# Optimization experiments

Hardware: AMD Instinct MI355X
Metric: run time of the kernel (lower is better)

Reference implementation:

```python
import jax, jax.numpy as jnp
import numpy as np

B, H, N, D, C, G = 4, 4, 4096, 256, 256, 64  # batch, heads, tokens, emb, channels, grid
EPS = 1e-5


def _layernorm(x, g, b):
    mu = jnp.mean(x, axis=-1, keepdims=True)
    var = jnp.var(x, axis=-1, keepdims=True)
    return (x - mu) * jax.lax.rsqrt(var + EPS) * g + b


def setup_inputs() -> dict:
    key = jax.random.key(0)
    ks = jax.random.split(key, 24)
    s = lambda fan_in: 1.0 / np.sqrt(fan_in)
    inp = {
        "img_emb": jax.random.normal(ks[0], (B, C, G, G), jnp.float32),
        "point_emb": jax.random.normal(ks[1], (B, N, D), jnp.float32),
        # stacked per-head projections (torch Linear: y = x @ W.T + b; store W already transposed)
        "Wq": jax.random.uniform(ks[2], (H, D, D), jnp.float32, -s(D), s(D)),
        "bq": jax.random.uniform(ks[3], (H, D), jnp.float32, -s(D), s(D)),
        "Wk": jax.random.uniform(ks[4], (H, C, D), jnp.float32, -s(C), s(C)),
        "bk": jax.random.uniform(ks[5], (H, D), jnp.float32, -s(C), s(C)),
        "Wv": jax.random.uniform(ks[6], (H, C, D), jnp.float32, -s(C), s(C)),
        "bv": jax.random.uniform(ks[7], (H, D), jnp.float32, -s(C), s(C)),
        "Wo": jax.random.uniform(ks[8], (H * D, D), jnp.float32, -s(H * D), s(H * D)),
        "bo": jax.random.uniform(ks[9], (D,), jnp.float32, -s(H * D), s(H * D)),
        "pos": jax.random.normal(ks[10], (N, D), jnp.float32),
        # FF: 256->128->64->1
        "W1": jax.random.uniform(ks[11], (256, 128), jnp.float32, -s(256), s(256)),
        "b1": jax.random.uniform(ks[12], (128,), jnp.float32, -s(256), s(256)),
        "g1": jnp.ones((128,), jnp.float32),
        "be1": jnp.zeros((128,), jnp.float32),
        "W2": jax.random.uniform(ks[13], (128, 64), jnp.float32, -s(128), s(128)),
        "b2": jax.random.uniform(ks[14], (64,), jnp.float32, -s(128), s(128)),
        "g2": jnp.ones((64,), jnp.float32),
        "be2": jnp.zeros((64,), jnp.float32),
        "W3": jax.random.uniform(ks[15], (64, 1), jnp.float32, -s(64), s(64)),
        "b3": jax.random.uniform(ks[16], (1,), jnp.float32, -s(64), s(64)),
    }
    return inp


def reference(img_emb, point_emb, Wq, bq, Wk, bk, Wv, bv, Wo, bo, pos,
              W1, b1, g1, be1, W2, b2, g2, be2, W3, b3):
    b = img_emb.shape[0]
    # [B, C, G, G] -> [B, N, C]
    img = jnp.transpose(img_emb, (0, 2, 3, 1)).reshape(b, -1, img_emb.shape[1])
    img_pos = img + pos[None, :, :]
    # batched per-head QKV (collapses the per-head Python loop)
    q = jnp.einsum('bnd,hde->bhne', point_emb, Wq) + bq[None, :, None, :]
    k = jnp.einsum('bnc,hce->bhne', img, Wk) + bk[None, :, None, :]
    v = jnp.einsum('bnc,hce->bhne', img_pos, Wv) + bv[None, :, None, :]
    scores = jnp.einsum('bhqe,bhke->bhqk', q, k) / jnp.sqrt(jnp.float32(D))
    attn = jax.nn.softmax(scores, axis=-1)
    att = jnp.einsum('bhqk,bhke->bhqe', attn, v)          # [B, H, N, E]
    att = jnp.transpose(att, (0, 2, 1, 3)).reshape(b, N, H * D)  # concat heads
    emb = att @ Wo + bo + point_emb                        # residual, [B, N, D]
    # small FFN head
    h = _layernorm(jax.nn.relu(emb @ W1 + b1), g1, be1)
    h = _layernorm(jax.nn.relu(h @ W2 + b2), g2, be2)
    act = jax.nn.sigmoid(h @ W3 + b3)                      # [B, N, 1]
    return act, emb
```

## Files before the change

### kernel.cpp

```cpp
#include <hip/hip_runtime.h>

typedef __attribute__((ext_vector_type(8))) short bfrag;
typedef __attribute__((ext_vector_type(8))) unsigned short us8;
typedef __attribute__((ext_vector_type(16))) float f16v;

__device__ __forceinline__ unsigned short f2bf(float f) {
  union { float f; unsigned u; } v; v.f = f;
  unsigned u = v.u;
  return (unsigned short)((u + 0x7fffu + ((u >> 16) & 1u)) >> 16);
}
__device__ __forceinline__ unsigned pkbf(float a, float b) {
  return (unsigned)f2bf(a) | ((unsigned)f2bf(b) << 16);
}
__device__ __forceinline__ float wred(float v) {
#pragma unroll
  for (int m = 32; m >= 1; m >>= 1) v += __shfl_xor(v, m, 64);
  return v;
}
__device__ __forceinline__ void dma16(const void* g, void* l) {
  __builtin_amdgcn_global_load_lds(
      (const __attribute__((address_space(1))) void*)g,
      (__attribute__((address_space(3))) void*)l, 16, 0, 0);
}

__device__ __forceinline__ void transp64(
    const float* __restrict__ inz, unsigned short* __restrict__ oz,
    int R, int Cc, int i0, int j0, int tid)
{
  int l = tid & 63, ty = tid >> 6;
  int i = i0 + l;
#pragma unroll
  for (int itr = 0; itr < 2; ++itr) {
    int j = j0 + ty * 16 + itr * 8;
    const float* p = inz + (long)i * Cc + j;
    float4 v0 = *(const float4*)(p);
    float4 v1 = *(const float4*)(p + 4);
    float vv[8] = {v0.x, v0.y, v0.z, v0.w, v1.x, v1.y, v1.z, v1.w};
#pragma unroll
    for (int s = 0; s < 8; ++s) oz[(long)(j + s) * R + i] = f2bf(vv[s]);
  }
}

__global__ __launch_bounds__(256) void prep_kernel(
    const float* __restrict__ point_emb, short* __restrict__ peT,
    const float* __restrict__ img_emb, const float* __restrict__ pos,
    short* __restrict__ imgT, short* __restrict__ imgPosT,
    const float* __restrict__ Wq, const float* __restrict__ Wk,
    const float* __restrict__ Wv, short* __restrict__ WqT,
    const float* __restrict__ Wo, short* __restrict__ WoT)
{
  __shared__ float tile[64][65];
  int b = blockIdx.x;
  int tid = threadIdx.x;

  if (b < 2048) {
    long i = ((long)b * 256 + tid) * 8;
    float4 v0 = *(const float4*)(point_emb + i);
    float4 v1 = *(const float4*)(point_emb + i + 4);
    uint4 st;
    st.x = pkbf(v0.x, v0.y);
    st.y = pkbf(v0.z, v0.w);
    st.z = pkbf(v1.x, v1.y);
    st.w = pkbf(v1.z, v1.w);
    *(uint4*)((unsigned short*)peT + i) = st;
  } else if (b < 3072) {
    int bb = b - 2048;
    int x = bb & 63, y = (bb >> 6) & 3, z = bb >> 8;
    long zofs = (long)z * (256L * 4096L);
    const float* inz = img_emb + zofs;
    int i0 = y * 64, j0 = x * 64;
    int r0 = (tid >> 6) * 16, c = tid & 63;
#pragma unroll
    for (int rr = 0; rr < 16; ++rr) {
      tile[c][r0 + rr] = inz[(long)(i0 + r0 + rr) * 4096 + j0 + c];
    }
    __syncthreads();
    unsigned short* o1 = (unsigned short*)imgT + zofs;
    unsigned short* o2 = (unsigned short*)imgPosT + zofs;
#pragma unroll
    for (int rr = 0; rr < 16; ++rr) {
      int tt = r0 + rr;
      float v = tile[tt][c];
      long o = (long)(j0 + tt) * 256 + i0 + c;
      o1[o] = f2bf(v);
      o2[o] = f2bf(v + pos[o]);
    }
  } else if (b < 3264) {
    int bb = b - 3072;
    int x = bb & 3, y = (bb >> 2) & 3, z = bb >> 4;
    const float* inz = (z < 4 ? Wq : (z < 8 ? Wk : Wv)) + (long)(z & 3) * 65536;
    unsigned short* oz = (unsigned short*)WqT + (long)z * 65536;
    transp64(inz, oz, 256, 256, x * 64, y * 64, tid);
  } else {
    int bb = b - 3264;
    int x = bb & 15, y = bb >> 4;
    transp64(Wo, (unsigned short*)WoT, 1024, 256, x * 64, y * 64, tid);
  }
}

__global__ __launch_bounds__(256) void gemm_qkv(
    const short* __restrict__ A, const short* __restrict__ Bt,
    const float* __restrict__ bias, short* __restrict__ Co,
    float scale, int transC)
{
  int id = blockIdx.x;
  int y = id & 3, h = (id >> 2) & 3;
  int g = id >> 4;
  int xt = g & 31, bsel = g >> 5;
  int z = bsel * 4 + h;

  const short* Az = A + (long)bsel * 1048576;
  const short* Btz = Bt + (long)h * 65536;
  const float* biasz = bias + (long)h * 256;
  short* Cz = Co + (long)z * 1048576;

  int tid = threadIdx.x;
  int w = tid >> 6, lane = tid & 63;
  int half = lane >> 5, ln = lane & 31;
  int wm = w & 1, wn = w >> 1;
  int row0 = xt * 128 + wm * 64;
  int col0 = y * 64 + wn * 32;

  f16v acc0, acc1;
#pragma unroll
  for (int i = 0; i < 16; ++i) { acc0[i] = 0.f; acc1[i] = 0.f; }

  const short* ap0 = Az + (long)(row0 + ln) * 256 + half * 8;
  const short* ap1 = Az + (long)(row0 + 32 + ln) * 256 + half * 8;
  const short* bp  = Btz + (long)(col0 + ln) * 256 + half * 8;

#pragma unroll
  for (int kt = 0; kt < 16; ++kt) {
    bfrag a0 = *(const bfrag*)(ap0 + kt * 16);
    bfrag a1 = *(const bfrag*)(ap1 + kt * 16);
    bfrag bb = *(const bfrag*)(bp + kt * 16);
    acc0 = __builtin_amdgcn_mfma_f32_32x32x16_bf16(a0, bb, acc0, 0, 0, 0);
    acc1 = __builtin_amdgcn_mfma_f32_32x32x16_bf16(a1, bb, acc1, 0, 0, 0);
  }

  int col = col0 + ln;
  float bv = biasz[col];
  if (transC) {
#pragma unroll
    for (int t = 0; t < 2; ++t) {
      int rbase = row0 + t * 32;
#pragma unroll
      for (int g2 = 0; g2 < 4; ++g2) {
        float v0 = ((t ? acc1[4*g2+0] : acc0[4*g2+0]) + bv) * scale;
        float v1 = ((t ? acc1[4*g2+1] : acc0[4*g2+1]) + bv) * scale;
        float v2 = ((t ? acc1[4*g2+2] : acc0[4*g2+2]) + bv) * scale;
        float v3 = ((t ? acc1[4*g2+3] : acc0[4*g2+3]) + bv) * scale;
        uint2 st;
        st.x = pkbf(v0, v1);
        st.y = pkbf(v2, v3);
        *(uint2*)&((unsigned short*)Cz)[(long)col * 4096 + rbase + 8 * g2 + 4 * half] = st;
      }
    }
  } else {
#pragma unroll
    for (int t = 0; t < 2; ++t) {
      int rbase = row0 + t * 32;
#pragma unroll
      for (int r = 0; r < 16; ++r) {
        float av = t ? acc1[r] : acc0[r];
        int rr = rbase + (r & 3) + 8 * (r >> 2) + 4 * half;
        ((unsigned short*)Cz)[(long)rr * 256 + col] = f2bf((av + bv) * scale);
      }
    }
  }
}

__global__ __launch_bounds__(256) void gemm_out(
    const short* __restrict__ A, const short* __restrict__ Bt,
    const float* __restrict__ bias, float* __restrict__ Co,
    const float* __restrict__ resid)
{
  int id = blockIdx.x;
  int xt = id >> 2, y = id & 3;

  int tid = threadIdx.x;
  int w = tid >> 6, lane = tid & 63;
  int half = lane >> 5, ln = lane & 31;
  int wm = w & 1, wn = w >> 1;
  int row0 = xt * 128 + wm * 64;
  int col0 = y * 64 + wn * 32;

  f16v acc0, acc1;
#pragma unroll
  for (int i = 0; i < 16; ++i) { acc0[i] = 0.f; acc1[i] = 0.f; }

  int r0 = row0 + ln, r1 = row0 + 32 + ln;
  long a0base = (long)(r0 >> 12) * 4194304 + (long)(r0 & 4095) * 256 + half * 8;
  long a1base = (long)(r1 >> 12) * 4194304 + (long)(r1 & 4095) * 256 + half * 8;
  const short* bp = Bt + (long)(col0 + ln) * 1024 + half * 8;

  for (int kh = 0; kh < 4; ++kh) {
    const short* a0p = A + a0base + (long)kh * 1048576;
    const short* a1p = A + a1base + (long)kh * 1048576;
    const short* bkp = bp + kh * 256;
#pragma unroll
    for (int kt = 0; kt < 16; ++kt) {
      bfrag a0 = *(const bfrag*)(a0p + kt * 16);
      bfrag a1 = *(const bfrag*)(a1p + kt * 16);
      bfrag bb = *(const bfrag*)(bkp + kt * 16);
      acc0 = __builtin_amdgcn_mfma_f32_32x32x16_bf16(a0, bb, acc0, 0, 0, 0);
      acc1 = __builtin_amdgcn_mfma_f32_32x32x16_bf16(a1, bb, acc1, 0, 0, 0);
    }
  }

  int col = col0 + ln;
  float bv = bias[col];
#pragma unroll
  for (int t = 0; t < 2; ++t) {
    int rbase = row0 + t * 32;
#pragma unroll
    for (int r = 0; r < 16; ++r) {
      float av = t ? acc1[r] : acc0[r];
      int rr = rbase + (r & 3) + 8 * (r >> 2) + 4 * half;
      Co[(long)rr * 256 + col] = av + bv + resid[(long)rr * 256 + col];
    }
  }
}

__global__ __launch_bounds__(512, 2) void attn_kernel(
    const short* __restrict__ Qg, const short* __restrict__ Kg,
    const short* __restrict__ Vtg, short* __restrict__ attc)
{
  __shared__ char smem[65536];
  int bx = blockIdx.x;
  int bh = bx & 15, qg = bx >> 4;
  int tid = threadIdx.x;
  int w = tid >> 6, lane = tid & 63;
  int half = lane >> 5, ln = lane & 31;
  int q0 = qg * 256 + w * 32;

  bfrag qf[16];
  {
    const short* qrow = Qg + ((long)bh * 4096 + q0 + ln) * 256 + half * 8;
#pragma unroll
    for (int kt = 0; kt < 16; ++kt) qf[kt] = *(const bfrag*)(qrow + kt * 16);
  }

  int koff[4], voff[2];
#pragma unroll
  for (int m = 0; m < 4; ++m) koff[m] = ((ln ^ (2 * m + half)) * 16) + half * 512;
#pragma unroll
  for (int kp = 0; kp < 2; ++kp) {
    int ck = 2 * kp + half;
    voff[kp] = 16384 + ck * 4096 + ((ln ^ (ck << 1)) * 16);
  }

  int w2 = w * 2;
  int kgl0, kgl1, vgl0, vgl1;
  {
    int c0 = w2 * 2 + half;
    kgl0 = (ln ^ (c0 & 7)) * 512 + c0 * 16;
    int c1 = (w2 + 1) * 2 + half;
    kgl1 = (ln ^ (c1 & 7)) * 512 + c1 * 16;
    int ck0 = w2 >> 2;
    int e0 = ((w2 & 3) * 64 + lane) ^ (ck0 << 1);
    vgl0 = e0 * 8192 + ck0 * 16;
    int ck1 = (w2 + 1) >> 2;
    int e1 = (((w2 + 1) & 3) * 64 + lane) ^ (ck1 << 1);
    vgl1 = e1 * 8192 + ck1 * 16;
  }
  const char* kgp = (const char*)Kg + (long)bh * 2097152;
  const char* vgp = (const char*)Vtg + (long)bh * 2097152;

  f16v O[8];
#pragma unroll
  for (int t = 0; t < 8; ++t)
#pragma unroll
    for (int r = 0; r < 16; ++r) O[t][r] = 0.f;

  float l_run = 0.f;
  union { bfrag f; unsigned u[4]; } bb[2];

#define PACK_BB(kp)                                                            \
  {                                                                            \
    unsigned q0_, q1_, q2_, q3_;                                               \
    asm("v_cvt_pk_bf16_f32 %0, %1, %2"                                         \
        : "=v"(q0_) : "v"(S[8*(kp)+0]), "v"(S[8*(kp)+1]));                     \
    asm("v_cvt_pk_bf16_f32 %0, %1, %2"                                         \
        : "=v"(q1_) : "v"(S[8*(kp)+2]), "v"(S[8*(kp)+3]));                     \
    asm("v_cvt_pk_bf16_f32 %0, %1, %2"                                         \
        : "=v"(q2_) : "v"(S[8*(kp)+4]), "v"(S[8*(kp)+5]));                     \
    asm("v_cvt_pk_bf16_f32 %0, %1, %2"                                         \
        : "=v"(q3_) : "v"(S[8*(kp)+6]), "v"(S[8*(kp)+7]));                     \
    asm("v_permlane32_swap_b32 %0, %1" : "+v"(q0_), "+v"(q2_));                \
    asm("v_permlane32_swap_b32 %0, %1" : "+v"(q1_), "+v"(q3_));                \
    bb[kp].u[0] = q0_;                                                         \
    bb[kp].u[1] = q1_;                                                         \
    bb[kp].u[2] = q2_;                                                         \
    bb[kp].u[3] = q3_;                                                         \
  }

  dma16(kgp + kgl0, smem + w2 * 1024);
  dma16(kgp + kgl1, smem + (w2 + 1) * 1024);
  kgp += 16384;

  __syncthreads();
  dma16(kgp + kgl0, smem + 32768 + w2 * 1024);
  dma16(kgp + kgl1, smem + 32768 + (w2 + 1) * 1024);
  kgp += 16384;
  dma16(vgp + vgl0, smem + 32768 + 16384 + w2 * 1024);
  dma16(vgp + vgl1, smem + 32768 + 16384 + (w2 + 1) * 1024);
  vgp += 64;
  {
    f16v S;
#pragma unroll
    for (int r = 0; r < 16; ++r) S[r] = 0.f;
#pragma unroll
    for (int kt = 0; kt < 16; ++kt) {
      bfrag a = *(const bfrag*)(smem + koff[kt & 3] + kt * 1024);
      S = __builtin_amdgcn_mfma_f32_32x32x16_bf16(a, qf[kt], S, 0, 0, 0);
    }
    float ss = 0.f;
#pragma unroll
    for (int r = 0; r < 16; ++r) { float e = exp2f(S[r] - 8.f); S[r] = e; ss += e; }
    l_run += ss;
    PACK_BB(0)
    PACK_BB(1)
  }

#define ATTN_ITER(BUF, KLOAD)                                                  \
  {                                                                            \
    __syncthreads();                                                           \
    if (KLOAD) {                                                               \
      dma16(kgp + kgl0, smem + ((BUF) ^ 1) * 32768 + w2 * 1024);               \
      dma16(kgp + kgl1, smem + ((BUF) ^ 1) * 32768 + (w2 + 1) * 1024);         \
      kgp += 16384;                                                            \
    }                                                                          \
    dma16(vgp + vgl0, smem + ((BUF) ^ 1) * 32768 + 16384 + w2 * 1024);         \
    dma16(vgp + vgl1, smem + ((BUF) ^ 1) * 32768 + 16384 + (w2 + 1) * 1024);   \
    vgp += 64;                                                                 \
    f16v S;                                                                    \
    _Pragma("unroll")                                                          \
    for (int r = 0; r < 16; ++r) S[r] = 0.f;                                   \
    _Pragma("unroll")                                                          \
    for (int kt = 0; kt < 16; ++kt) {                                          \
      bfrag a = *(const bfrag*)(smem + koff[kt & 3] + ((BUF)*32768 + kt*1024));\
      S = __builtin_amdgcn_mfma_f32_32x32x16_bf16(a, qf[kt], S, 0, 0, 0);      \
      bfrag va = *(const bfrag*)(smem + voff[kt >> 3] +                        \
                                 ((BUF)*32768 + (kt & 7) * 512));              \
      O[kt & 7] = __builtin_amdgcn_mfma_f32_32x32x16_bf16(va, bb[kt >> 3].f,   \
                                                          O[kt & 7], 0, 0, 0); \
    }                                                                          \
    float ss = 0.f;                                                            \
    _Pragma("unroll")                                                          \
    for (int r = 0; r < 16; ++r) { float e = exp2f(S[r] - 8.f); S[r] = e; ss += e; } \
    l_run += ss;                                                               \
    PACK_BB(0)                                                                 \
    PACK_BB(1)                                                                 \
  }

  for (int tp = 0; tp < 63; ++tp) {
    ATTN_ITER(1, 1)
    ATTN_ITER(0, 1)
  }
  ATTN_ITER(1, 0)
#undef ATTN_ITER

  __syncthreads();
#pragma unroll
  for (int kp = 0; kp < 2; ++kp) {
#pragma unroll
    for (int mt = 0; mt < 8; ++mt) {
      bfrag va = *(const bfrag*)(smem + voff[kp] + mt * 512);
      O[mt] = __builtin_amdgcn_mfma_f32_32x32x16_bf16(va, bb[kp].f, O[mt], 0, 0, 0);
    }
  }
#undef PACK_BB

  l_run += __shfl_xor(l_run, 32);
  float rl = 1.0f / l_run;
  short* orow = attc + ((long)bh * 4096 + q0 + ln) * 256;
#pragma unroll
  for (int mt = 0; mt < 8; ++mt) {
#pragma unroll
    for (int g = 0; g < 4; ++g) {
      uint2 st;
      st.x = pkbf(O[mt][4 * g + 0] * rl, O[mt][4 * g + 1] * rl);
      st.y = pkbf(O[mt][4 * g + 2] * rl, O[mt][4 * g + 3] * rl);
      *(uint2*)(orow + mt * 32 + 8 * g + 4 * half) = st;
    }
  }
}

__global__ __launch_bounds__(256) void ffn_kernel(
    const float* __restrict__ emb,
    const float* __restrict__ W1, const float* __restrict__ b1,
    const float* __restrict__ g1, const float* __restrict__ be1,
    const float* __restrict__ W2, const float* __restrict__ b2,
    const float* __restrict__ g2, const float* __restrict__ be2,
    const float* __restrict__ W3, const float* __restrict__ b3,
    float* __restrict__ act)
{
  __shared__ float xs[4][256][4];
  __shared__ float hs[4][128][4];
  int w = threadIdx.x >> 6, l = threadIdx.x & 63;
  int row0 = blockIdx.x * 16 + w * 4;
  const float* x = emb + (long)row0 * 256;

  {
    float xv[4][4];
#pragma unroll
    for (int rr = 0; rr < 4; ++rr) {
      float4 t = *(const float4*)(x + rr * 256 + 4 * l);
      xv[0][rr] = t.x; xv[1][rr] = t.y; xv[2][rr] = t.z; xv[3][rr] = t.w;
    }
#pragma unroll
    for (int i = 0; i < 4; ++i) {
      float4 st = make_float4(xv[i][0], xv[i][1], xv[i][2], xv[i][3]);
      *(float4*)&xs[w][4 * l + i][0] = st;
    }
  }

  float a0[4], a1[4];
  {
    float bb0 = b1[2 * l], bb1 = b1[2 * l + 1];
#pragma unroll
    for (int rr = 0; rr < 4; ++rr) { a0[rr] = bb0; a1[rr] = bb1; }
  }
  for (int k = 0; k < 256; ++k) {
    float w0 = W1[k * 128 + 2 * l], w1 = W1[k * 128 + 2 * l + 1];
    float4 xv = *(const float4*)&xs[w][k][0];
    a0[0] += xv.x * w0; a1[0] += xv.x * w1;
    a0[1] += xv.y * w0; a1[1] += xv.y * w1;
    a0[2] += xv.z * w0; a1[2] += xv.z * w1;
    a0[3] += xv.w * w0; a1[3] += xv.w * w1;
  }
  {
    float gg0 = g1[2 * l], gg1 = g1[2 * l + 1];
    float ee0 = be1[2 * l], ee1 = be1[2 * l + 1];
    float n0v[4], n1v[4];
#pragma unroll
    for (int rr = 0; rr < 4; ++rr) {
      float u0 = fmaxf(a0[rr], 0.f), u1 = fmaxf(a1[rr], 0.f);
      float s1 = wred(u0 + u1);
      float s2 = wred(u0 * u0 + u1 * u1);
      float mu = s1 * (1.f / 128.f);
      float var = fmaxf(s2 * (1.f / 128.f) - mu * mu, 0.f);
      float rs = rsqrtf(var + 1e-5f);
      n0v[rr] = (u0 - mu) * rs * gg0 + ee0;
      n1v[rr] = (u1 - mu) * rs * gg1 + ee1;
    }
    *(float4*)&hs[w][2 * l][0]     = make_float4(n0v[0], n0v[1], n0v[2], n0v[3]);
    *(float4*)&hs[w][2 * l + 1][0] = make_float4(n1v[0], n1v[1], n1v[2], n1v[3]);
  }

  float c0[4];
  {
    float bb2 = b2[l];
#pragma unroll
    for (int rr = 0; rr < 4; ++rr) c0[rr] = bb2;
  }
  for (int k = 0; k < 128; ++k) {
    float w2 = W2[k * 64 + l];
    float4 hv = *(const float4*)&hs[w][k][0];
    c0[0] += hv.x * w2;
    c0[1] += hv.y * w2;
    c0[2] += hv.z * w2;
    c0[3] += hv.w * w2;
  }
  {
    float gg2 = g2[l], ee2 = be2[l], w3 = W3[l], bb3 = b3[0];
#pragma unroll
    for (int rr = 0; rr < 4; ++rr) {
      float u = fmaxf(c0[rr], 0.f);
      float t1 = wred(u);
      float t2 = wred(u * u);
      float mu2 = t1 * (1.f / 64.f);
      float var2 = fmaxf(t2 * (1.f / 64.f) - mu2 * mu2, 0.f);
      float rs2 = rsqrtf(var2 + 1e-5f);
      float n2 = (u - mu2) * rs2 * gg2 + ee2;
      float tt = wred(n2 * w3);
      if (l == 0) {
        float r = tt + bb3;
        act[row0 + rr] = 1.f / (1.f + __expf(-r));
      }
    }
  }
}

extern "C" void kernel_launch(void* const* d_in, const int* in_sizes, int n_in,
                              void* d_out, int out_size, void* d_ws, size_t ws_size,
                              hipStream_t stream)
{
  const float* img_emb   = (const float*)d_in[0];
  const float* point_emb = (const float*)d_in[1];
  const float* Wq = (const float*)d_in[2];
  const float* bq = (const float*)d_in[3];
  const float* Wk = (const float*)d_in[4];
  const float* bk = (const float*)d_in[5];
  const float* Wv = (const float*)d_in[6];
  const float* bv = (const float*)d_in[7];
  const float* Wo = (const float*)d_in[8];
  const float* bo = (const float*)d_in[9];
  const float* pos = (const float*)d_in[10];
  const float* W1 = (const float*)d_in[11];
  const float* b1 = (const float*)d_in[12];
  const float* g1 = (const float*)d_in[13];
  const float* be1 = (const float*)d_in[14];
  const float* W2 = (const float*)d_in[15];
  const float* b2 = (const float*)d_in[16];
  const float* g2 = (const float*)d_in[17];
  const float* be2 = (const float*)d_in[18];
  const float* W3 = (const float*)d_in[19];
  const float* b3 = (const float*)d_in[20];

  char* ws = (char*)d_ws;
  short* Qb      = (short*)(ws + 0);
  short* Kb      = (short*)(ws + 33554432);
  short* VtB     = (short*)(ws + 67108864);
  short* peT     = (short*)(ws + 67108864);
  short* imgT    = (short*)(ws + 75497472);
  short* imgPosT = (short*)(ws + 100663296);
  short* WoT     = (short*)(ws + 109051904);
  short* WqT     = (short*)(ws + 109576192);
  short* WkT     = (short*)(ws + 110100480);
  short* WvT     = (short*)(ws + 110624768);
  (void)WkT; (void)WvT;

  float* act_out = (float*)d_out;
  float* emb_out = (float*)d_out + 16384;

  const float qscale = 0.0901684400555602f;

  prep_kernel<<<3328, 256, 0, stream>>>(point_emb, peT, img_emb, pos,
                                        imgT, imgPosT, Wq, Wk, Wv, WqT, Wo, WoT);

  gemm_qkv<<<2048, 256, 0, stream>>>(peT, WqT, bq, Qb, qscale, 0);
  gemm_qkv<<<2048, 256, 0, stream>>>(imgT, WqT + 262144, bk, Kb, 1.0f, 0);
  gemm_qkv<<<2048, 256, 0, stream>>>(imgPosT, WqT + 524288, bv, VtB, 1.0f, 1);

  attn_kernel<<<256, 512, 0, stream>>>(Qb, Kb, VtB, Qb);

  gemm_out<<<512, 256, 0, stream>>>(Qb, WoT, bo, emb_out, point_emb);

  ffn_kernel<<<1024, 256, 0, stream>>>(emb_out, W1, b1, g1, be1, W2, b2, g2, be2,
                                       W3, b3, act_out);
}
```

Baseline: 631.5 us.

## Software-pipeline attention scores with softmax; merge Q and K projection launches

The attention loop is restructured so the QK^T MFMA chain for the current key tile runs before the softmax and bf16 packing of the previous tile's scores. Two score accumulators alternate between iterations, which lets the exp work overlap with matrix work. To free registers for the second accumulator, half of the Q fragments move into a doubled 128KB shared-memory buffer and are re-read from LDS on every iteration, adding LDS traffic. Separately, the Q and K projection GEMMs are fused into one launch and the V projection becomes its own kernel with the transposed store only.

```diff
diff --git a/kernel.cpp b/kernel.cpp
--- a/kernel.cpp
+++ b/kernel.cpp
@@ -98,12 +98,22 @@
   }
 }
 
-__global__ __launch_bounds__(256) void gemm_qkv(
-    const short* __restrict__ A, const short* __restrict__ Bt,
-    const float* __restrict__ bias, short* __restrict__ Co,
-    float scale, int transC)
-{
-  int id = blockIdx.x;
+__global__ __launch_bounds__(256) void gemm_qk(
+    const short* __restrict__ Aq, const short* __restrict__ Btq,
+    const float* __restrict__ biasq, short* __restrict__ Cq,
+    const short* __restrict__ Ak, const short* __restrict__ Btk,
+    const float* __restrict__ biask, short* __restrict__ Ck,
+    float qscale)
+{
+  int idg = blockIdx.x;
+  int sel = idg >> 11;
+  int id = idg & 2047;
+  const short* A  = sel ? Ak : Aq;
+  const short* Bt = sel ? Btk : Btq;
+  const float* bias = sel ? biask : biasq;
+  short* Co = sel ? Ck : Cq;
+  float scale = sel ? 1.0f : qscale;
+
   int y = id & 3, h = (id >> 2) & 3;
   int g = id >> 4;
   int xt = g & 31, bsel = g >> 5;
@@ -133,50 +143,39 @@
   for (int kt = 0; kt < 16; ++kt) {
     bfrag a0 = *(const bfrag*)(ap0 + kt * 16);
     bfrag a1 = *(const bfrag*)(ap1 + kt * 16);
-    bfrag bb = *(const bfrag*)(bp + kt * 16);
-    acc0 = __builtin_amdgcn_mfma_f32_32x32x16_bf16(a0, bb, acc0, 0, 0, 0);
-    acc1 = __builtin_amdgcn_mfma_f32_32x32x16_bf16(a1, bb, acc1, 0, 0, 0);
+    bfrag bbv = *(const bfrag*)(bp + kt * 16);
+    acc0 = __builtin_amdgcn_mfma_f32_32x32x16_bf16(a0, bbv, acc0, 0, 0, 0);
+    acc1 = __builtin_amdgcn_mfma_f32_32x32x16_bf16(a1, bbv, acc1, 0, 0, 0);
   }
 
   int col = col0 + ln;
   float bv = biasz[col];
-  if (transC) {
-#pragma unroll
-    for (int t = 0; t < 2; ++t) {
-      int rbase = row0 + t * 32;
-#pragma unroll
-      for (int g2 = 0; g2 < 4; ++g2) {
-        float v0 = ((t ? acc1[4*g2+0] : acc0[4*g2+0]) + bv) * scale;
-        float v1 = ((t ? acc1[4*g2+1] : acc0[4*g2+1]) + bv) * scale;
-        float v2 = ((t ? acc1[4*g2+2] : acc0[4*g2+2]) + bv) * scale;
-        float v3 = ((t ? acc1[4*g2+3] : acc0[4*g2+3]) + bv) * scale;
-        uint2 st;
-        st.x = pkbf(v0, v1);
-        st.y = pkbf(v2, v3);
-        *(uint2*)&((unsigned short*)Cz)[(long)col * 4096 + rbase + 8 * g2 + 4 * half] = st;
-      }
-    }
-  } else {
-#pragma unroll
-    for (int t = 0; t < 2; ++t) {
-      int rbase = row0 + t * 32;
-#pragma unroll
-      for (int r = 0; r < 16; ++r) {
-        float av = t ? acc1[r] : acc0[r];
-        int rr = rbase + (r & 3) + 8 * (r >> 2) + 4 * half;
-        ((unsigned short*)Cz)[(long)rr * 256 + col] = f2bf((av + bv) * scale);
-      }
-    }
-  }
-}
-
-__global__ __launch_bounds__(256) void gemm_out(
+#pragma unroll
+  for (int t = 0; t < 2; ++t) {
+    int rbase = row0 + t * 32;
+#pragma unroll
+    for (int r = 0; r < 16; ++r) {
+      float av = t ? acc1[r] : acc0[r];
+      int rr = rbase + (r & 3) + 8 * (r >> 2) + 4 * half;
+      ((unsigned short*)Cz)[(long)rr * 256 + col] = f2bf((av + bv) * scale);
+    }
+  }
+}
+
+__global__ __launch_bounds__(256) void gemm_v(
     const short* __restrict__ A, const short* __restrict__ Bt,
-    const float* __restrict__ bias, float* __restrict__ Co,
-    const float* __restrict__ resid)
+    const float* __restrict__ bias, short* __restrict__ Co)
 {
   int id = blockIdx.x;
-  int xt = id >> 2, y = id & 3;
+  int y = id & 3, h = (id >> 2) & 3;
+  int g = id >> 4;
+  int xt = g & 31, bsel = g >> 5;
+  int z = bsel * 4 + h;
+
+  const short* Az = A + (long)bsel * 1048576;
+  const short* Btz = Bt + (long)h * 65536;
+  const float* biasz = bias + (long)h * 256;
+  short* Cz = Co + (long)z * 1048576;
 
   int tid = threadIdx.x;
   int w = tid >> 6, lane = tid & 63;
@@ -189,6 +188,57 @@
 #pragma unroll
   for (int i = 0; i < 16; ++i) { acc0[i] = 0.f; acc1[i] = 0.f; }
 
+  const short* ap0 = Az + (long)(row0 + ln) * 256 + half * 8;
+  const short* ap1 = Az + (long)(row0 + 32 + ln) * 256 + half * 8;
+  const short* bp  = Btz + (long)(col0 + ln) * 256 + half * 8;
+
+#pragma unroll
+  for (int kt = 0; kt < 16; ++kt) {
+    bfrag a0 = *(const bfrag*)(ap0 + kt * 16);
+    bfrag a1 = *(const bfrag*)(ap1 + kt * 16);
+    bfrag bbv = *(const bfrag*)(bp + kt * 16);
+    acc0 = __builtin_amdgcn_mfma_f32_32x32x16_bf16(a0, bbv, acc0, 0, 0, 0);
+    acc1 = __builtin_amdgcn_mfma_f32_32x32x16_bf16(a1, bbv, acc1, 0, 0, 0);
+  }
+
+  int col = col0 + ln;
+  float bv = biasz[col];
+#pragma unroll
+  for (int t = 0; t < 2; ++t) {
+    int rbase = row0 + t * 32;
+#pragma unroll
+    for (int g2 = 0; g2 < 4; ++g2) {
+      float v0 = (t ? acc1[4*g2+0] : acc0[4*g2+0]) + bv;
+      float v1 = (t ? acc1[4*g2+1] : acc0[4*g2+1]) + bv;
+      float v2 = (t ? acc1[4*g2+2] : acc0[4*g2+2]) + bv;
+      float v3 = (t ? acc1[4*g2+3] : acc0[4*g2+3]) + bv;
+      uint2 st;
+      st.x = pkbf(v0, v1);
+      st.y = pkbf(v2, v3);
+      *(uint2*)&((unsigned short*)Cz)[(long)col * 4096 + rbase + 8 * g2 + 4 * half] = st;
+    }
+  }
+}
+
+__global__ __launch_bounds__(256) void gemm_out(
+    const short* __restrict__ A, const short* __restrict__ Bt,
+    const float* __restrict__ bias, float* __restrict__ Co,
+    const float* __restrict__ resid)
+{
+  int id = blockIdx.x;
+  int xt = id >> 2, y = id & 3;
+
+  int tid = threadIdx.x;
+  int w = tid >> 6, lane = tid & 63;
+  int half = lane >> 5, ln = lane & 31;
+  int wm = w & 1, wn = w >> 1;
+  int row0 = xt * 128 + wm * 64;
+  int col0 = y * 64 + wn * 32;
+
+  f16v acc0, acc1;
+#pragma unroll
+  for (int i = 0; i < 16; ++i) { acc0[i] = 0.f; acc1[i] = 0.f; }
+
   int r0 = row0 + ln, r1 = row0 + 32 + ln;
   long a0base = (long)(r0 >> 12) * 4194304 + (long)(r0 & 4095) * 256 + half * 8;
   long a1base = (long)(r1 >> 12) * 4194304 + (long)(r1 & 4095) * 256 + half * 8;
@@ -202,9 +252,9 @@
     for (int kt = 0; kt < 16; ++kt) {
       bfrag a0 = *(const bfrag*)(a0p + kt * 16);
       bfrag a1 = *(const bfrag*)(a1p + kt * 16);
-      bfrag bb = *(const bfrag*)(bkp + kt * 16);
-      acc0 = __builtin_amdgcn_mfma_f32_32x32x16_bf16(a0, bb, acc0, 0, 0, 0);
-      acc1 = __builtin_amdgcn_mfma_f32_32x32x16_bf16(a1, bb, acc1, 0, 0, 0);
+      bfrag bbv = *(const bfrag*)(bkp + kt * 16);
+      acc0 = __builtin_amdgcn_mfma_f32_32x32x16_bf16(a0, bbv, acc0, 0, 0, 0);
+      acc1 = __builtin_amdgcn_mfma_f32_32x32x16_bf16(a1, bbv, acc1, 0, 0, 0);
     }
   }
 
@@ -226,7 +276,7 @@
     const short* __restrict__ Qg, const short* __restrict__ Kg,
     const short* __restrict__ Vtg, short* __restrict__ attc)
 {
-  __shared__ char smem[65536];
+  __shared__ char smem[131072];
   int bx = blockIdx.x;
   int bh = bx & 15, qg = bx >> 4;
   int tid = threadIdx.x;
@@ -234,11 +284,17 @@
   int half = lane >> 5, ln = lane & 31;
   int q0 = qg * 256 + w * 32;
 
-  bfrag qf[16];
+  bfrag qf[8];
+  int qoff = 65536 + w * 8192 + lane * 16;
   {
     const short* qrow = Qg + ((long)bh * 4096 + q0 + ln) * 256 + half * 8;
 #pragma unroll
-    for (int kt = 0; kt < 16; ++kt) qf[kt] = *(const bfrag*)(qrow + kt * 16);
+    for (int kt = 0; kt < 8; ++kt) qf[kt] = *(const bfrag*)(qrow + kt * 16);
+#pragma unroll
+    for (int kt = 8; kt < 16; ++kt) {
+      us8 v = *(const us8*)(qrow + kt * 16);
+      *(us8*)(smem + qoff + (kt - 8) * 1024) = v;
+    }
   }
 
   int koff[4], voff[2];
@@ -275,24 +331,52 @@
 
   float l_run = 0.f;
   union { bfrag f; unsigned u[4]; } bb[2];
-
-#define PACK_BB(kp)                                                            \
+  f16v SA, SB;
+
+#define PACK_BB(kp, SV)                                                        \
   {                                                                            \
     unsigned q0_, q1_, q2_, q3_;                                               \
     asm("v_cvt_pk_bf16_f32 %0, %1, %2"                                         \
-        : "=v"(q0_) : "v"(S[8*(kp)+0]), "v"(S[8*(kp)+1]));                     \
+        : "=v"(q0_) : "v"(SV[8*(kp)+0]), "v"(SV[8*(kp)+1]));                   \
     asm("v_cvt_pk_bf16_f32 %0, %1, %2"                                         \
-        : "=v"(q1_) : "v"(S[8*(kp)+2]), "v"(S[8*(kp)+3]));                     \
+        : "=v"(q1_) : "v"(SV[8*(kp)+2]), "v"(SV[8*(kp)+3]));                   \
     asm("v_cvt_pk_bf16_f32 %0, %1, %2"                                         \
-        : "=v"(q2_) : "v"(S[8*(kp)+4]), "v"(S[8*(kp)+5]));                     \
+        : "=v"(q2_) : "v"(SV[8*(kp)+4]), "v"(SV[8*(kp)+5]));                   \
     asm("v_cvt_pk_bf16_f32 %0, %1, %2"                                         \
-        : "=v"(q3_) : "v"(S[8*(kp)+6]), "v"(S[8*(kp)+7]));                     \
+        : "=v"(q3_) : "v"(SV[8*(kp)+6]), "v"(SV[8*(kp)+7]));                   \
     asm("v_permlane32_swap_b32 %0, %1" : "+v"(q0_), "+v"(q2_));                \
     asm("v_permlane32_swap_b32 %0, %1" : "+v"(q1_), "+v"(q3_));                \
     bb[kp].u[0] = q0_;                                                         \
     bb[kp].u[1] = q1_;                                                         \
     bb[kp].u[2] = q2_;                                                         \
     bb[kp].u[3] = q3_;                                                         \
+  }
+
+#define SOFTMAX_BB(SV)                                                         \
+  {                                                                            \
+    float ss = 0.f;                                                            \
+    _Pragma("unroll")                                                          \
+    for (int r = 0; r < 16; ++r) { float e = exp2f(SV[r] - 8.f); SV[r] = e; ss += e; } \
+    l_run += ss;                                                               \
+    PACK_BB(0, SV)                                                             \
+    PACK_BB(1, SV)                                                             \
+  }
+
+#define SCHAIN(BUF, SNEW)                                                      \
+  {                                                                            \
+    _Pragma("unroll")                                                          \
+    for (int r = 0; r < 16; ++r) SNEW[r] = 0.f;                                \
+    _Pragma("unroll")                                                          \
+    for (int kt = 0; kt < 8; ++kt) {                                           \
+      bfrag a = *(const bfrag*)(smem + koff[kt & 3] + ((BUF)*32768 + kt*1024));\
+      SNEW = __builtin_amdgcn_mfma_f32_32x32x16_bf16(a, qf[kt], SNEW, 0, 0, 0);\
+    }                                                                          \
+    _Pragma("unroll")                                                          \
+    for (int kt = 8; kt < 16; ++kt) {                                          \
+      bfrag a = *(const bfrag*)(smem + koff[kt & 3] + ((BUF)*32768 + kt*1024));\
+      bfrag qv = *(const bfrag*)(smem + qoff + (kt - 8) * 1024);               \
+      SNEW = __builtin_amdgcn_mfma_f32_32x32x16_bf16(a, qv, SNEW, 0, 0, 0);    \
+    }                                                                          \
   }
 
   dma16(kgp + kgl0, smem + w2 * 1024);
@@ -306,24 +390,9 @@
   dma16(vgp + vgl0, smem + 32768 + 16384 + w2 * 1024);
   dma16(vgp + vgl1, smem + 32768 + 16384 + (w2 + 1) * 1024);
   vgp += 64;
-  {
-    f16v S;
-#pragma unroll
-    for (int r = 0; r < 16; ++r) S[r] = 0.f;
-#pragma unroll
-    for (int kt = 0; kt < 16; ++kt) {
-      bfrag a = *(const bfrag*)(smem + koff[kt & 3] + kt * 1024);
-      S = __builtin_amdgcn_mfma_f32_32x32x16_bf16(a, qf[kt], S, 0, 0, 0);
-    }
-    float ss = 0.f;
-#pragma unroll
-    for (int r = 0; r < 16; ++r) { float e = exp2f(S[r] - 8.f); S[r] = e; ss += e; }
-    l_run += ss;
-    PACK_BB(0)
-    PACK_BB(1)
-  }
-
-#define ATTN_ITER(BUF, KLOAD)                                                  \
+  SCHAIN(0, SB)
+
+#define ATTN_ITER(BUF, KLOAD, SNEW, SPREV)                                     \
   {                                                                            \
     __syncthreads();                                                           \
     if (KLOAD) {                                                               \
@@ -334,34 +403,25 @@
     dma16(vgp + vgl0, smem + ((BUF) ^ 1) * 32768 + 16384 + w2 * 1024);         \
     dma16(vgp + vgl1, smem + ((BUF) ^ 1) * 32768 + 16384 + (w2 + 1) * 1024);   \
     vgp += 64;                                                                 \
-    f16v S;                                                                    \
-    _Pragma("unroll")                                                          \
-    for (int r = 0; r < 16; ++r) S[r] = 0.f;                                   \
+    SCHAIN(BUF, SNEW)                                                          \
+    SOFTMAX_BB(SPREV)                                                          \
     _Pragma("unroll")                                                          \
     for (int kt = 0; kt < 16; ++kt) {                                          \
-      bfrag a = *(const bfrag*)(smem + koff[kt & 3] + ((BUF)*32768 + kt*1024));\
-      S = __builtin_amdgcn_mfma_f32_32x32x16_bf16(a, qf[kt], S, 0, 0, 0);      \
       bfrag va = *(const bfrag*)(smem + voff[kt >> 3] +                        \
                                  ((BUF)*32768 + (kt & 7) * 512));              \
       O[kt & 7] = __builtin_amdgcn_mfma_f32_32x32x16_bf16(va, bb[kt >> 3].f,   \
                                                           O[kt & 7], 0, 0, 0); \
     }                                                                          \
-    float ss = 0.f;                                                            \
-    _Pragma("unroll")                                                          \
-    for (int r = 0; r < 16; ++r) { float e = exp2f(S[r] - 8.f); S[r] = e; ss += e; } \
-    l_run += ss;                                                               \
-    PACK_BB(0)                                                                 \
-    PACK_BB(1)                                                                 \
   }
 
   for (int tp = 0; tp < 63; ++tp) {
-    ATTN_ITER(1, 1)
-    ATTN_ITER(0, 1)
-  }
-  ATTN_ITER(1, 0)
-#undef ATTN_ITER
+    ATTN_ITER(1, 1, SA, SB)
+    ATTN_ITER(0, 1, SB, SA)
+  }
+  ATTN_ITER(1, 0, SA, SB)
 
   __syncthreads();
+  SOFTMAX_BB(SA)
 #pragma unroll
   for (int kp = 0; kp < 2; ++kp) {
 #pragma unroll
@@ -370,6 +430,9 @@
       O[mt] = __builtin_amdgcn_mfma_f32_32x32x16_bf16(va, bb[kp].f, O[mt], 0, 0, 0);
     }
   }
+#undef ATTN_ITER
+#undef SCHAIN
+#undef SOFTMAX_BB
 #undef PACK_BB
 
   l_run += __shfl_xor(l_run, 32);
@@ -530,9 +593,9 @@
   prep_kernel<<<3328, 256, 0, stream>>>(point_emb, peT, img_emb, pos,
                                         imgT, imgPosT, Wq, Wk, Wv, WqT, Wo, WoT);
 
-  gemm_qkv<<<2048, 256, 0, stream>>>(peT, WqT, bq, Qb, qscale, 0);
-  gemm_qkv<<<2048, 256, 0, stream>>>(imgT, WqT + 262144, bk, Kb, 1.0f, 0);
-  gemm_qkv<<<2048, 256, 0, stream>>>(imgPosT, WqT + 524288, bv, VtB, 1.0f, 1);
+  gemm_qk<<<4096, 256, 0, stream>>>(peT, WqT, bq, Qb,
+                                    imgT, WqT + 262144, bk, Kb, qscale);
+  gemm_v<<<2048, 256, 0, stream>>>(imgPosT, WqT + 524288, bv, VtB);
 
   attn_kernel<<<256, 512, 0, stream>>>(Qb, Kb, VtB, Qb);
 
```

Result: faster. 611.9 us (median of 2 runs) (-3.1%).
